# Optimization experiments

Measured on AMD Instinct MI355X. Metric: run time of the kernel, lower is better.

The kernel has to match this reference:

```python
import jax, jax.numpy as jnp
import numpy as np

EPS = np.float32(np.finfo(float).eps)  # 2.220446049250313e-16, matches torch code
TOP_K = 2


def setup_inputs() -> dict:
    key = jax.random.key(0)
    ks = jax.random.split(key, 7)
    B, D, H, E = 8192, 1024, 4096, 8
    # init scales mirror the torch MLP init (std = sqrt(2/(m+n)), sqrt(1/m))
    return {
        "inp": jax.random.normal(ks[0], (B, D), dtype=jnp.float32),
        "gate_w": jax.random.normal(ks[1], (E, D), dtype=jnp.float32) * np.sqrt(1.0 / D).astype(np.float32),
        "gate_b": jax.random.normal(ks[2], (E,), dtype=jnp.float32) * 0.01,
        "W1": jax.random.normal(ks[3], (E, H, D), dtype=jnp.float32) * np.sqrt(2.0 / (H + D)).astype(np.float32),
        "b1": jax.random.normal(ks[4], (E, H), dtype=jnp.float32) * np.sqrt(1.0 / H).astype(np.float32),
        "W2": jax.random.normal(ks[5], (E, D, H), dtype=jnp.float32) * np.sqrt(2.0 / (D + H)).astype(np.float32),
        "b2": jax.random.normal(ks[6], (E, D), dtype=jnp.float32) * np.sqrt(1.0 / D).astype(np.float32),
    }


def _moe_forward(inp, gate_w, gate_b, W1, b1, W2, b2):
    B = inp.shape[0]
    E = gate_w.shape[0]
    # --- NaiveGate: linear -> top-k -> softmax -> scatter into dense gates ---
    logits = inp @ gate_w.T + gate_b                      # [B, E]
    top_vals, top_idx = jax.lax.top_k(logits, TOP_K)      # [B, k]
    top_gates = jax.nn.softmax(top_vals, axis=-1)         # top_k > 1 branch
    gates = jnp.zeros((B, E), dtype=jnp.float32)
    gates = gates.at[jnp.arange(B)[:, None], top_idx].set(top_gates)

    # --- Experts: 2-layer MLP, ReLU after every linear (sigmoid_layer=-1) ---
    h = jax.nn.relu(jnp.einsum('bd,ehd->ebh', inp, W1) + b1[:, None, :])   # [E, B, H]
    out = jax.nn.relu(jnp.einsum('ebh,edh->ebd', h, W2) + b2[:, None, :])  # [E, B, D]

    # --- SparseDispatcher.combine: exp -> gate-weighted scatter-sum -> +eps -> log ---
    # Dense-equivalent: gates are exactly zero for non-routed (token, expert)
    # pairs, so the weighted sum matches the sparse scatter exactly.
    combined = jnp.einsum('be,ebd->bd', gates, jnp.exp(out))
    return jnp.log(combined + EPS)


def reference(inp, gate_w, gate_b, W1, b1, W2, b2):
    return _moe_forward(inp, gate_w, gate_b, W1, b1, W2, b2)
```

## Files before the change

kernel.cpp:

```cpp
#include <hip/hip_runtime.h>
#include <hip/hip_bf16.h>
#include <math.h>

#define B_TOK 8192
#define DDIM  1024
#define HDIM  4096
#define NEXP  8
#define CAP   17408

typedef unsigned short u16;
using f32x4  = __attribute__((ext_vector_type(4))) float;
using bf16x8 = __attribute__((ext_vector_type(8))) short;
using u16x8  = __attribute__((ext_vector_type(8))) unsigned short;

__device__ __forceinline__ u16 f2bf(float f) {
  union { float f; unsigned u; } v; v.f = f;
  unsigned r = v.u + 0x7FFFu + ((v.u >> 16) & 1u);
  return (u16)(r >> 16);
}

__device__ __forceinline__ void load_lds16(const void* g, void* l) {
  __builtin_amdgcn_global_load_lds((const __attribute__((address_space(1))) void*)g,
                                   (__attribute__((address_space(3))) void*)l,
                                   16, 0, 0);
}

__global__ __launch_bounds__(256) void prep_kernel(
    const float* __restrict__ inp, const float* __restrict__ gw,
    const float* __restrict__ gb, int* __restrict__ tok_e,
    float* __restrict__ tok_g, int* __restrict__ counts,
    ushort4* __restrict__ Xb4,
    const float* __restrict__ w1, const float* __restrict__ w2,
    u16* __restrict__ w1b, u16* __restrict__ w2b, int n8each)
{
  if (blockIdx.x >= 2048) {
    const int wb   = blockIdx.x - 2048;
    const int half = wb >> 11;
    const int lb   = wb & 2047;
    const f32x4* src = (const f32x4*)(half ? w2 : w1);
    u16x8*       dst = (u16x8*)(half ? w2b : w1b);
    const int tcnt = 2048 * 256;
    const int base = lb * 256 + threadIdx.x;
    for (int o = 0; o < n8each; o += 4 * tcnt) {
      f32x4 a[4][2];
#pragma unroll
      for (int k = 0; k < 4; ++k) {
        int i = base + o + k * tcnt;
        if (i < n8each) {
          a[k][0] = src[2 * i];
          a[k][1] = src[2 * i + 1];
        }
      }
#pragma unroll
      for (int k = 0; k < 4; ++k) {
        int i = base + o + k * tcnt;
        if (i < n8each) {
          u16x8 v;
          v[0] = f2bf(a[k][0][0]); v[1] = f2bf(a[k][0][1]);
          v[2] = f2bf(a[k][0][2]); v[3] = f2bf(a[k][0][3]);
          v[4] = f2bf(a[k][1][0]); v[5] = f2bf(a[k][1][1]);
          v[6] = f2bf(a[k][1][2]); v[7] = f2bf(a[k][1][3]);
          __builtin_nontemporal_store(v, &dst[i]);
        }
      }
    }
    return;
  }
  int gtid = blockIdx.x * 256 + threadIdx.x;
  int tok  = gtid >> 6;
  int lane = threadIdx.x & 63;
  if (tok >= B_TOK) return;
  const float4* X = (const float4*)(inp + (size_t)tok * DDIM);
  float4 x[4];
#pragma unroll
  for (int j = 0; j < 4; ++j) x[j] = X[j * 64 + lane];
  ushort4* Xrow = Xb4 + (size_t)tok * (DDIM / 4);
#pragma unroll
  for (int j = 0; j < 4; ++j) {
    ushort4 o;
    o.x = f2bf(x[j].x); o.y = f2bf(x[j].y); o.z = f2bf(x[j].z); o.w = f2bf(x[j].w);
    Xrow[j * 64 + lane] = o;
  }
  float lg[NEXP];
#pragma unroll
  for (int e = 0; e < NEXP; ++e) {
    const float4* W = (const float4*)(gw + e * DDIM);
    double s = 0.0;
#pragma unroll
    for (int j = 0; j < 4; ++j) {
      float4 w = W[j * 64 + lane];
      s += (double)x[j].x * w.x + (double)x[j].y * w.y
         + (double)x[j].z * w.z + (double)x[j].w * w.w;
    }
#pragma unroll
    for (int o = 32; o > 0; o >>= 1) s += __shfl_xor(s, o);
    lg[e] = (float)(s + (double)gb[e]);
  }
  if (lane == 0) {
    int i0 = 0; float v0 = lg[0];
#pragma unroll
    for (int e = 1; e < NEXP; ++e) if (lg[e] > v0) { v0 = lg[e]; i0 = e; }
    int i1 = -1; float v1 = -3.4e38f;
#pragma unroll
    for (int e = 0; e < NEXP; ++e) if (e != i0 && lg[e] > v1) { v1 = lg[e]; i1 = e; }
    float t   = __expf(v1 - v0);
    float inv = 1.0f / (1.0f + t);
    tok_e[2 * tok] = i0; tok_e[2 * tok + 1] = i1;
    tok_g[2 * tok] = inv; tok_g[2 * tok + 1] = t * inv;
    atomicAdd(&counts[i0], 1);
    atomicAdd(&counts[i1], 1);
  }
}

__global__ __launch_bounds__(256) void scatter_kernel(
    const int* __restrict__ tok_e, const float* __restrict__ tok_g,
    const int* __restrict__ counts, int* __restrict__ cursors,
    int* __restrict__ slot_token, float* __restrict__ slot_gate,
    int* __restrict__ tok_slot,
    int* __restrict__ offs, int* __restrict__ padded)
{
  __shared__ int soffs[NEXP];
  if (threadIdx.x == 0) {
    int off = 0;
    for (int e = 0; e < NEXP; ++e) {
      soffs[e] = off;
      int p = (counts[e] + 127) & ~127;
      off += p;
      if (blockIdx.x == 0) { offs[e] = soffs[e]; padded[e] = p; }
    }
  }
  __syncthreads();
  int b = blockIdx.x * 256 + threadIdx.x;
  if (b >= B_TOK) return;
#pragma unroll
  for (int k = 0; k < 2; ++k) {
    int e   = tok_e[2 * b + k];
    float g = tok_g[2 * b + k];
    int pos = atomicAdd(&cursors[e], 1);
    int s   = soffs[e] + pos;
    slot_token[s] = b;
    slot_gate[s]  = g;
    tok_slot[2 * b + k] = s;
  }
}

#define STAGE(kt_) do {                                                   \
    _Pragma("unroll") for (int g = 0; g < 4; ++g) {                       \
      load_lds16(pAg[g] + (kt_) * 64, &As[(g * 256 + tid) * 8]);           \
      load_lds16(pBg[g] + (kt_) * 64, &Bs[(g * 256 + tid) * 8]);           \
    } } while (0)

#define GEMM_BODY(NT_) do {                                               \
    const int NT = (NT_);                                                 \
    _Pragma("unroll 1")                                                   \
    for (int t = 0; t < NT; ++t) {                                        \
      STAGE(t);                                                           \
      __syncthreads();                                                    \
      bf16x8 af[4][2], bfr[4][2];                                         \
      _Pragma("unroll") for (int m = 0; m < 4; ++m)                       \
        _Pragma("unroll") for (int kk = 0; kk < 2; ++kk)                  \
          af[m][kk] = *(const bf16x8*)&As[(wm + m*16 + fr)*64             \
                                        + (((kk*4 + fq) ^ fr7) * 8)];     \
      _Pragma("unroll") for (int n = 0; n < 4; ++n)                       \
        _Pragma("unroll") for (int kk = 0; kk < 2; ++kk)                  \
          bfr[n][kk] = *(const bf16x8*)&Bs[(wn + n*16 + fr)*64            \
                                        + (((kk*4 + fq) ^ fr7) * 8)];     \
      _Pragma("unroll") for (int kk = 0; kk < 2; ++kk)                    \
      _Pragma("unroll") for (int m = 0; m < 4; ++m)                       \
      _Pragma("unroll") for (int n = 0; n < 4; ++n)                       \
        acc[m][n] = __builtin_amdgcn_mfma_f32_16x16x32_bf16(              \
            af[m][kk], bfr[n][kk], acc[m][n], 0, 0, 0);                   \
      __syncthreads();                                                    \
    } } while (0)

__global__ __launch_bounds__(256, 4) void gemm1_kernel(
    const u16* __restrict__ Xb, const u16* __restrict__ W1b,
    const float* __restrict__ b1, const int* __restrict__ slot_token,
    const int* __restrict__ offs, const int* __restrict__ padded,
    u16* __restrict__ Hb)
{
  const int h   = blockIdx.x + 32 * (blockIdx.y + 64 * blockIdx.z);
  const int e   = h & 7;
  const int r   = h >> 3;
  const int mi  = r >> 5;
  const int nti = r & 31;
  if (mi * 128 >= padded[e]) return;
  const int base_slot = offs[e] + mi * 128;
  const int n0 = nti * 128;

  __shared__ __align__(16) u16 As[8192];
  __shared__ __align__(16) u16 Bs[8192];
  __shared__ int toks[128];

  const int tid = threadIdx.x;
  if (tid < 128) toks[tid] = slot_token[base_slot + tid];
  __syncthreads();

  const u16* pAg[4];
  const u16* pBg[4];
#pragma unroll
  for (int g = 0; g < 4; ++g) {
    int i = g * 256 + tid, rr = i >> 3, sl = i & 7;
    int kc = (sl ^ (rr & 7)) * 8;
    pAg[g] = Xb + (size_t)toks[rr] * DDIM + kc;
    pBg[g] = W1b + ((size_t)e * HDIM + (size_t)(n0 + rr)) * DDIM + kc;
  }

  const int wave = tid >> 6, lane = tid & 63;
  const int wm = (wave >> 1) * 64, wn = (wave & 1) * 64;
  const int fr = lane & 15, fq = lane >> 4, fr7 = fr & 7;

  f32x4 acc[4][4];
#pragma unroll
  for (int m = 0; m < 4; ++m)
#pragma unroll
    for (int n = 0; n < 4; ++n) acc[m][n] = f32x4{0.f, 0.f, 0.f, 0.f};

  GEMM_BODY(DDIM / 64);

#pragma unroll
  for (int n = 0; n < 4; ++n) {
    int col = n0 + wn + n * 16 + fr;
    float bias = b1[e * HDIM + col];
#pragma unroll
    for (int m = 0; m < 4; ++m) {
      int row0 = wm + m * 16 + fq * 4;
#pragma unroll
      for (int j = 0; j < 4; ++j) {
        float v = acc[m][n][j] + bias;
        v = v > 0.f ? v : 0.f;
        Hb[(size_t)(base_slot + row0 + j) * HDIM + col] = f2bf(v);
      }
    }
  }
}

__global__ __launch_bounds__(256, 4) void gemm2_kernel(
    const u16* __restrict__ Hb, const u16* __restrict__ W2b,
    const float* __restrict__ b2, const float* __restrict__ slot_gate,
    const int* __restrict__ offs, const int* __restrict__ padded,
    float* __restrict__ P)
{
  const int h   = blockIdx.x + 8 * (blockIdx.y + 64 * blockIdx.z);
  const int e   = h & 7;
  const int r   = h >> 3;
  const int mi  = r >> 3;
  const int nti = r & 7;
  if (mi * 128 >= padded[e]) return;
  const int base_slot = offs[e] + mi * 128;
  const int n0 = nti * 128;

  __shared__ __align__(16) u16 As[8192];
  __shared__ __align__(16) u16 Bs[8192];
  __shared__ float gts[128];

  const int tid = threadIdx.x;
  if (tid < 128) gts[tid] = slot_gate[base_slot + tid];
  __syncthreads();

  const u16* pAg[4];
  const u16* pBg[4];
#pragma unroll
  for (int g = 0; g < 4; ++g) {
    int i = g * 256 + tid, rr = i >> 3, sl = i & 7;
    int kc = (sl ^ (rr & 7)) * 8;
    pAg[g] = Hb + (size_t)(base_slot + rr) * HDIM + kc;
    pBg[g] = W2b + ((size_t)e * DDIM + (size_t)(n0 + rr)) * HDIM + kc;
  }

  const int wave = tid >> 6, lane = tid & 63;
  const int wm = (wave >> 1) * 64, wn = (wave & 1) * 64;
  const int fr = lane & 15, fq = lane >> 4, fr7 = fr & 7;

  f32x4 acc[4][4];
#pragma unroll
  for (int m = 0; m < 4; ++m)
#pragma unroll
    for (int n = 0; n < 4; ++n) acc[m][n] = f32x4{0.f, 0.f, 0.f, 0.f};

  GEMM_BODY(HDIM / 64);

#pragma unroll
  for (int n = 0; n < 4; ++n) {
    int col = n0 + wn + n * 16 + fr;
    float bias = b2[e * DDIM + col];
#pragma unroll
    for (int m = 0; m < 4; ++m) {
      int row0 = wm + m * 16 + fq * 4;
#pragma unroll
      for (int j = 0; j < 4; ++j) {
        int row = row0 + j;
        float v = acc[m][n][j] + bias;
        v = v > 0.f ? v : 0.f;
        P[(size_t)(base_slot + row) * DDIM + col] = gts[row] * __expf(v);
      }
    }
  }
}

__global__ __launch_bounds__(256) void combine_kernel(
    const float4* __restrict__ P4, const int* __restrict__ tok_slot,
    float4* __restrict__ out4)
{
  const float EPS = 2.220446049250313e-16f;
  const int total = B_TOK * (DDIM / 4);
  for (int i = blockIdx.x * 256 + threadIdx.x; i < total; i += gridDim.x * 256) {
    int tok = i >> 8, d4 = i & 255;
    int s0 = tok_slot[2 * tok], s1 = tok_slot[2 * tok + 1];
    float4 a = P4[(size_t)s0 * (DDIM / 4) + d4];
    float4 b = P4[(size_t)s1 * (DDIM / 4) + d4];
    float4 v;
    v.x = logf(a.x + b.x + EPS);
    v.y = logf(a.y + b.y + EPS);
    v.z = logf(a.z + b.z + EPS);
    v.w = logf(a.w + b.w + EPS);
    out4[i] = v;
  }
}

extern "C" void kernel_launch(void* const* d_in, const int* in_sizes, int n_in,
                              void* d_out, int out_size, void* d_ws, size_t ws_size,
                              hipStream_t stream)
{
  const float* inp = (const float*)d_in[0];
  const float* gw  = (const float*)d_in[1];
  const float* gb  = (const float*)d_in[2];
  const float* W1  = (const float*)d_in[3];
  const float* b1  = (const float*)d_in[4];
  const float* W2  = (const float*)d_in[5];
  const float* b2  = (const float*)d_in[6];
  float* out = (float*)d_out;

  char* ws = (char*)d_ws;
  size_t off = 0;
  auto alloc = [&](size_t bytes) {
    void* p = ws + off;
    off = (off + bytes + 255) & ~(size_t)255;
    return p;
  };
  u16*   Xb  = (u16*)alloc((size_t)B_TOK * DDIM * 2);
  u16*   W1b = (u16*)alloc((size_t)NEXP * HDIM * DDIM * 2);
  float* P   = (float*)Xb;
  u16*   W2b = (u16*)alloc((size_t)NEXP * DDIM * HDIM * 2);
  u16*   Hb  = (u16*)alloc((size_t)CAP * HDIM * 2);
  int*   slot_token = (int*)alloc(CAP * 4);
  float* slot_gate  = (float*)alloc(CAP * 4);
  int*   tok_e    = (int*)alloc(B_TOK * 2 * 4);
  float* tok_g    = (float*)alloc(B_TOK * 2 * 4);
  int*   tok_slot = (int*)alloc(B_TOK * 2 * 4);
  int*   counts  = (int*)alloc(32);
  int*   cursors = (int*)alloc(32);
  int*   offs    = (int*)alloc(32);
  int*   padded  = (int*)alloc(32);

  (void)hipMemsetAsync(counts, 0, 288, stream);
  (void)hipMemsetAsync(slot_token, 0, (size_t)CAP * 8, stream);

  prep_kernel<<<6144, 256, 0, stream>>>(inp, gw, gb, tok_e, tok_g, counts,
                                        (ushort4*)Xb,
                                        W1, W2, W1b, W2b,
                                        NEXP * HDIM * DDIM / 8);
  scatter_kernel<<<B_TOK / 256, 256, 0, stream>>>(tok_e, tok_g, counts, cursors,
                                                  slot_token, slot_gate, tok_slot,
                                                  offs, padded);

  gemm1_kernel<<<dim3(32, 64, NEXP), 256, 0, stream>>>(
      Xb, W1b, b1, slot_token, offs, padded, Hb);
  gemm2_kernel<<<dim3(8, 64, NEXP), 256, 0, stream>>>(
      Hb, W2b, b2, slot_gate, offs, padded, P);

  combine_kernel<<<2048, 256, 0, stream>>>((const float4*)P, tok_slot, (float4*)out);
}
```

Baseline: 694.6 us.

## Overlap W2 bf16 conversion with gemm1 by moving it into extra grid slice

Moves the fp32-to-bf16 conversion of W2 out of the prep kernel and into a ninth z-slice of the gemm1 grid, so the memory-bound conversion can run alongside the compute-bound first expert GEMM. The prep kernel now converts only W1, which shortens the critical path before gemm1. Because the z==8 blocks sit at the end of the linear block order, they may be scheduled after most GEMM tiles and end up adding to gemm1's tail rather than overlapping. They also compete with the GEMM for bandwidth and CU slots.

```diff
diff --git a/kernel.cpp b/kernel.cpp
--- a/kernel.cpp
+++ b/kernel.cpp
@@ -25,45 +25,43 @@
                                    16, 0, 0);
 }
 
+__device__ __forceinline__ void cvt_stream(const float* __restrict__ src_,
+                                           u16* __restrict__ dst_,
+                                           int base, int tcnt, int n8) {
+  const f32x4* src = (const f32x4*)src_;
+  u16x8*       dst = (u16x8*)dst_;
+  for (int o = 0; o < n8; o += 4 * tcnt) {
+    f32x4 a[4][2];
+#pragma unroll
+    for (int k = 0; k < 4; ++k) {
+      int i = base + o + k * tcnt;
+      if (i < n8) { a[k][0] = src[2 * i]; a[k][1] = src[2 * i + 1]; }
+    }
+#pragma unroll
+    for (int k = 0; k < 4; ++k) {
+      int i = base + o + k * tcnt;
+      if (i < n8) {
+        u16x8 v;
+        v[0] = f2bf(a[k][0][0]); v[1] = f2bf(a[k][0][1]);
+        v[2] = f2bf(a[k][0][2]); v[3] = f2bf(a[k][0][3]);
+        v[4] = f2bf(a[k][1][0]); v[5] = f2bf(a[k][1][1]);
+        v[6] = f2bf(a[k][1][2]); v[7] = f2bf(a[k][1][3]);
+        __builtin_nontemporal_store(v, &dst[i]);
+      }
+    }
+  }
+}
+
 __global__ __launch_bounds__(256) void prep_kernel(
     const float* __restrict__ inp, const float* __restrict__ gw,
     const float* __restrict__ gb, int* __restrict__ tok_e,
     float* __restrict__ tok_g, int* __restrict__ counts,
     ushort4* __restrict__ Xb4,
-    const float* __restrict__ w1, const float* __restrict__ w2,
-    u16* __restrict__ w1b, u16* __restrict__ w2b, int n8each)
+    const float* __restrict__ w1, u16* __restrict__ w1b, int n8)
 {
   if (blockIdx.x >= 2048) {
-    const int wb   = blockIdx.x - 2048;
-    const int half = wb >> 11;
-    const int lb   = wb & 2047;
-    const f32x4* src = (const f32x4*)(half ? w2 : w1);
-    u16x8*       dst = (u16x8*)(half ? w2b : w1b);
-    const int tcnt = 2048 * 256;
-    const int base = lb * 256 + threadIdx.x;
-    for (int o = 0; o < n8each; o += 4 * tcnt) {
-      f32x4 a[4][2];
-#pragma unroll
-      for (int k = 0; k < 4; ++k) {
-        int i = base + o + k * tcnt;
-        if (i < n8each) {
-          a[k][0] = src[2 * i];
-          a[k][1] = src[2 * i + 1];
-        }
-      }
-#pragma unroll
-      for (int k = 0; k < 4; ++k) {
-        int i = base + o + k * tcnt;
-        if (i < n8each) {
-          u16x8 v;
-          v[0] = f2bf(a[k][0][0]); v[1] = f2bf(a[k][0][1]);
-          v[2] = f2bf(a[k][0][2]); v[3] = f2bf(a[k][0][3]);
-          v[4] = f2bf(a[k][1][0]); v[5] = f2bf(a[k][1][1]);
-          v[6] = f2bf(a[k][1][2]); v[7] = f2bf(a[k][1][3]);
-          __builtin_nontemporal_store(v, &dst[i]);
-        }
-      }
-    }
+    const int lb = blockIdx.x - 2048;
+    cvt_stream(w1, w1b, lb * 256 + threadIdx.x, 2048 * 256, n8);
     return;
   }
   int gtid = blockIdx.x * 256 + threadIdx.x;
@@ -177,8 +175,14 @@
     const u16* __restrict__ Xb, const u16* __restrict__ W1b,
     const float* __restrict__ b1, const int* __restrict__ slot_token,
     const int* __restrict__ offs, const int* __restrict__ padded,
-    u16* __restrict__ Hb)
-{
+    u16* __restrict__ Hb,
+    const float* __restrict__ w2, u16* __restrict__ w2b, int n8w2)
+{
+  if (blockIdx.z == 8) {
+    const int lb = blockIdx.x + 32 * blockIdx.y;
+    cvt_stream(w2, w2b, lb * 256 + (int)threadIdx.x, 2048 * 256, n8w2);
+    return;
+  }
   const int h   = blockIdx.x + 32 * (blockIdx.y + 64 * blockIdx.z);
   const int e   = h & 7;
   const int r   = h >> 3;
@@ -356,16 +360,16 @@
   (void)hipMemsetAsync(counts, 0, 288, stream);
   (void)hipMemsetAsync(slot_token, 0, (size_t)CAP * 8, stream);
 
-  prep_kernel<<<6144, 256, 0, stream>>>(inp, gw, gb, tok_e, tok_g, counts,
-                                        (ushort4*)Xb,
-                                        W1, W2, W1b, W2b,
-                                        NEXP * HDIM * DDIM / 8);
+  const int n8 = NEXP * HDIM * DDIM / 8;
+
+  prep_kernel<<<4096, 256, 0, stream>>>(inp, gw, gb, tok_e, tok_g, counts,
+                                        (ushort4*)Xb, W1, W1b, n8);
   scatter_kernel<<<B_TOK / 256, 256, 0, stream>>>(tok_e, tok_g, counts, cursors,
                                                   slot_token, slot_gate, tok_slot,
                                                   offs, padded);
 
-  gemm1_kernel<<<dim3(32, 64, NEXP), 256, 0, stream>>>(
-      Xb, W1b, b1, slot_token, offs, padded, Hb);
+  gemm1_kernel<<<dim3(32, 64, NEXP + 1), 256, 0, stream>>>(
+      Xb, W1b, b1, slot_token, offs, padded, Hb, W2, W2b, n8);
   gemm2_kernel<<<dim3(8, 64, NEXP), 256, 0, stream>>>(
       Hb, W2b, b2, slot_gate, offs, padded, P);
 
```

After: 708.4 us. Within noise of the previous version (+2.0%).
